# Optimization experiments

Hardware: AMD Instinct MI355X
Metric: run time of the kernel (lower is better)

The kernel has to match this reference:

```python
import jax, jax.numpy as jnp
import numpy as np

THRESHOLD = 0.1  # init kwarg
N_NODES = 8192
N_EDGES = 16384


def setup_inputs() -> dict:
    key = jax.random.key(0)
    k1, k2 = jax.random.split(key)
    node_pos = jax.random.normal(k1, (N_NODES, 2), dtype=jnp.float32)
    edge_index = jax.random.randint(k2, (2, N_EDGES), 0, N_NODES, dtype=jnp.int64)
    return {"node_pos": node_pos, "edge_index": edge_index}


def reference(node_pos, edge_index):
    # edge direction vectors, normalized to unit length (clamped norm as in torch)
    ev = node_pos[edge_index[1]] - node_pos[edge_index[0]]          # [E, 2]
    norms = jnp.linalg.norm(ev, axis=1, keepdims=True)
    ev = ev / jnp.clip(norms, 1e-6)
    # pairwise cosine of angle between every pair of edges: [E, E] gram matrix
    cos = ev @ ev.T
    mask = jnp.abs(cos) > THRESHOLD
    # original loops over i < j only: subtract diagonal hits, halve the rest
    diag_hits = jnp.sum(jnp.abs(jnp.diagonal(cos)) > THRESHOLD)
    n_edges = ev.shape[0]
    count = (jnp.sum(mask) - diag_hits).astype(jnp.float32) * 0.5
    return count / (n_edges * (n_edges - 1) / 2)
```

## Files before the change

kernel.cpp:

```cpp
#include <hip/hip_runtime.h>
#include <math.h>


#define K_BINS 8192
#define NTHR   1024
#define KPT    16
#define PI_F   3.14159265358979323846f
#define A_LO_F 1.4706289056333368f

__global__ __launch_bounds__(256) void angle_kernel(const float* __restrict__ pos,
                                                    const int* __restrict__ eidx,
                                                    float* __restrict__ phi, int E) {
    int i = blockIdx.x * blockDim.x + threadIdx.x;
    if (i >= E) return;
    int s = eidx[i];
    int t = eidx[E + i];
    float dx = pos[2 * t]     - pos[2 * s];
    float dy = pos[2 * t + 1] - pos[2 * s + 1];
    float p;
    if (dx == 0.f && dy == 0.f) {
        p = -1.f;
    } else {
        p = atan2f(dy, dx);
        if (p < 0.f)    p += PI_F;
        if (p >= PI_F)  p -= PI_F;
        if (p < 0.f)    p = 0.f;
    }
    phi[i] = p;
}

__global__ __launch_bounds__(NTHR) void hist_count_kernel(const float* __restrict__ phi,
                                                          float* __restrict__ out, int E) {
    __shared__ unsigned hist[K_BINS];
    __shared__ unsigned wbase[NTHR / 64];
    __shared__ unsigned long long wU[NTHR / 64];
    __shared__ unsigned wND[NTHR / 64];
    __shared__ unsigned s_total;

    int tid  = threadIdx.x;
    int lane = tid & 63;
    int wid  = tid >> 6;
    const float scale = (float)K_BINS / PI_F;

    for (int b = tid; b < K_BINS; b += NTHR) hist[b] = 0u;
    __syncthreads();

    float ph[KPT];
#pragma unroll
    for (int k = 0; k < KPT; ++k) {
        int i = tid + k * NTHR;
        float p = (i < E) ? phi[i] : -1.f;
        ph[k] = p;
        if (p >= 0.f) {
            int b = (int)(p * scale);
            if (b >= K_BINS) b = K_BINS - 1;
            atomicAdd(&hist[b], 1u);
        }
    }
    __syncthreads();

    unsigned h[8];
    unsigned lsum = 0;
    int base = tid * (K_BINS / NTHR);
#pragma unroll
    for (int k = 0; k < 8; ++k) { h[k] = hist[base + k]; lsum += h[k]; }
    unsigned inc = lsum;
    for (int off = 1; off < 64; off <<= 1) {
        unsigned v = __shfl_up(inc, off);
        if (lane >= off) inc += v;
    }
    if (lane == 63) wbase[wid] = inc;
    __syncthreads();
    if (tid < NTHR / 64) {
        unsigned wv = wbase[tid];
        unsigned winc = wv;
        for (int off = 1; off < NTHR / 64; off <<= 1) {
            unsigned v = __shfl_up(winc, off);
            if (tid >= off) winc += v;
        }
        wbase[tid] = winc - wv;
        if (tid == NTHR / 64 - 1) s_total = winc;
    }
    __syncthreads();
    unsigned run = wbase[wid] + (inc - lsum);
#pragma unroll
    for (int k = 0; k < 8; ++k) { hist[base + k] = run; run += h[k]; }
    __syncthreads();

    unsigned total = s_total;
    unsigned long long U = 0;
    unsigned nd = 0;
#pragma unroll
    for (int k = 0; k < KPT; ++k) {
        float p = ph[k];
        if (p < 0.f) continue;
        nd++;
        float lo = p + A_LO_F;
        float hi = p + (PI_F - A_LO_F);
        if (lo >= PI_F) lo -= PI_F;
        if (hi >= PI_F) hi -= PI_F;
        int blo = (int)(lo * scale); if (blo >= K_BINS) blo = K_BINS - 1;
        int bhi = (int)(hi * scale); if (bhi >= K_BINS) bhi = K_BINS - 1;
        unsigned c = (blo <= bhi) ? (hist[bhi] - hist[blo])
                                  : (total - hist[blo] + hist[bhi]);
        U += c;
    }
    for (int off = 32; off > 0; off >>= 1) {
        U  += __shfl_down(U, off);
        nd += __shfl_down(nd, off);
    }
    if (lane == 0) { wU[wid] = U; wND[wid] = nd; }
    __syncthreads();
    if (tid == 0) {
        unsigned long long Ut = 0; unsigned ndt = 0;
        for (int w = 0; w < NTHR / 64; ++w) { Ut += wU[w]; ndt += wND[w]; }
        double nd_d = (double)ndt;
        double pairs_nd  = nd_d * (nd_d - 1.0) * 0.5;
        double band_pairs = (double)Ut * 0.5;
        double count = pairs_nd - band_pairs;
        double denom = (double)E * (double)(E - 1) * 0.5;
        out[0] = (float)(count / denom);
    }
}

extern "C" void kernel_launch(void* const* d_in, const int* in_sizes, int n_in,
                              void* d_out, int out_size, void* d_ws, size_t ws_size,
                              hipStream_t stream) {
    const float* pos  = (const float*)d_in[0];
    const int*   eidx = (const int*)d_in[1];
    int E = in_sizes[1] / 2;

    float* phi = (float*)d_ws;

    angle_kernel<<<(E + 255) / 256, 256, 0, stream>>>(pos, eidx, phi, E);
    hist_count_kernel<<<1, NTHR, 0, stream>>>(phi, (float*)d_out, E);
}
```

Before: 66.16 us.

## Store quantized bin indices and count band pairs per bin instead of per edge

```diff
diff --git a/kernel.cpp b/kernel.cpp
--- a/kernel.cpp
+++ b/kernel.cpp
@@ -3,67 +3,74 @@
 
 
 #define K_BINS 8192
+#define OFF_LO 3835
+#define OFF_HI (K_BINS - OFF_LO)
 #define NTHR   1024
-#define KPT    16
+#define BPT    (K_BINS / NTHR)
 #define PI_F   3.14159265358979323846f
-#define A_LO_F 1.4706289056333368f
 
-__global__ __launch_bounds__(256) void angle_kernel(const float* __restrict__ pos,
-                                                    const int* __restrict__ eidx,
-                                                    float* __restrict__ phi, int E) {
+__global__ __launch_bounds__(64) void bin_kernel(const float* __restrict__ pos,
+                                                 const int* __restrict__ eidx,
+                                                 unsigned short* __restrict__ bins, int E) {
     int i = blockIdx.x * blockDim.x + threadIdx.x;
     if (i >= E) return;
     int s = eidx[i];
     int t = eidx[E + i];
     float dx = pos[2 * t]     - pos[2 * s];
     float dy = pos[2 * t + 1] - pos[2 * s + 1];
-    float p;
+    unsigned short b;
     if (dx == 0.f && dy == 0.f) {
-        p = -1.f;
+        b = 0xFFFFu;
     } else {
-        p = atan2f(dy, dx);
-        if (p < 0.f)    p += PI_F;
-        if (p >= PI_F)  p -= PI_F;
-        if (p < 0.f)    p = 0.f;
+        float p = atan2f(dy, dx);
+        if (p < 0.f)   p += PI_F;
+        int bi = (int)(p * ((float)K_BINS / PI_F));
+        if (bi >= K_BINS) bi -= K_BINS;
+        if (bi < 0) bi = 0;
+        b = (unsigned short)bi;
     }
-    phi[i] = p;
+    bins[i] = b;
 }
 
-__global__ __launch_bounds__(NTHR) void hist_count_kernel(const float* __restrict__ phi,
+__global__ __launch_bounds__(NTHR) void hist_count_kernel(const unsigned short* __restrict__ bins,
                                                           float* __restrict__ out, int E) {
     __shared__ unsigned hist[K_BINS];
     __shared__ unsigned wbase[NTHR / 64];
     __shared__ unsigned long long wU[NTHR / 64];
-    __shared__ unsigned wND[NTHR / 64];
     __shared__ unsigned s_total;
 
     int tid  = threadIdx.x;
     int lane = tid & 63;
     int wid  = tid >> 6;
-    const float scale = (float)K_BINS / PI_F;
 
     for (int b = tid; b < K_BINS; b += NTHR) hist[b] = 0u;
     __syncthreads();
 
-    float ph[KPT];
+    {
+        const uint4* v = (const uint4*)bins;
+        int nvec = E / 8;
 #pragma unroll
-    for (int k = 0; k < KPT; ++k) {
-        int i = tid + k * NTHR;
-        float p = (i < E) ? phi[i] : -1.f;
-        ph[k] = p;
-        if (p >= 0.f) {
-            int b = (int)(p * scale);
-            if (b >= K_BINS) b = K_BINS - 1;
-            atomicAdd(&hist[b], 1u);
+        for (int k = 0; k < 2; ++k) {
+            int idx = tid + k * NTHR;
+            if (idx < nvec) {
+                uint4 w = v[idx];
+                unsigned ws[4] = {w.x, w.y, w.z, w.w};
+#pragma unroll
+                for (int q = 0; q < 4; ++q) {
+                    unsigned lo = ws[q] & 0xFFFFu, hi = ws[q] >> 16;
+                    if (lo != 0xFFFFu) atomicAdd(&hist[lo], 1u);
+                    if (hi != 0xFFFFu) atomicAdd(&hist[hi], 1u);
+                }
+            }
         }
     }
     __syncthreads();
 
-    unsigned h[8];
+    unsigned h[BPT];
     unsigned lsum = 0;
-    int base = tid * (K_BINS / NTHR);
+    int base = tid * BPT;
 #pragma unroll
-    for (int k = 0; k < 8; ++k) { h[k] = hist[base + k]; lsum += h[k]; }
+    for (int k = 0; k < BPT; ++k) { h[k] = hist[base + k]; lsum += h[k]; }
     unsigned inc = lsum;
     for (int off = 1; off < 64; off <<= 1) {
         unsigned v = __shfl_up(inc, off);
@@ -84,40 +91,31 @@
     __syncthreads();
     unsigned run = wbase[wid] + (inc - lsum);
 #pragma unroll
-    for (int k = 0; k < 8; ++k) { hist[base + k] = run; run += h[k]; }
+    for (int k = 0; k < BPT; ++k) { hist[base + k] = run; run += h[k]; }
     __syncthreads();
 
     unsigned total = s_total;
     unsigned long long U = 0;
-    unsigned nd = 0;
 #pragma unroll
-    for (int k = 0; k < KPT; ++k) {
-        float p = ph[k];
-        if (p < 0.f) continue;
-        nd++;
-        float lo = p + A_LO_F;
-        float hi = p + (PI_F - A_LO_F);
-        if (lo >= PI_F) lo -= PI_F;
-        if (hi >= PI_F) hi -= PI_F;
-        int blo = (int)(lo * scale); if (blo >= K_BINS) blo = K_BINS - 1;
-        int bhi = (int)(hi * scale); if (bhi >= K_BINS) bhi = K_BINS - 1;
-        unsigned c = (blo <= bhi) ? (hist[bhi] - hist[blo])
-                                  : (total - hist[blo] + hist[bhi]);
-        U += c;
+    for (int k = 0; k < BPT; ++k) {
+        unsigned c = h[k];
+        if (c) {
+            int b  = base + k;
+            int xm = (b + OFF_LO) & (K_BINS - 1);
+            int ym = (b + OFF_HI) & (K_BINS - 1);
+            unsigned W = (xm < ym) ? (hist[ym] - hist[xm])
+                                   : (total - hist[xm] + hist[ym]);
+            U += (unsigned long long)c * W;
+        }
     }
-    for (int off = 32; off > 0; off >>= 1) {
-        U  += __shfl_down(U, off);
-        nd += __shfl_down(nd, off);
-    }
-    if (lane == 0) { wU[wid] = U; wND[wid] = nd; }
+    for (int off = 32; off > 0; off >>= 1) U += __shfl_down(U, off);
+    if (lane == 0) wU[wid] = U;
     __syncthreads();
     if (tid == 0) {
-        unsigned long long Ut = 0; unsigned ndt = 0;
-        for (int w = 0; w < NTHR / 64; ++w) { Ut += wU[w]; ndt += wND[w]; }
-        double nd_d = (double)ndt;
-        double pairs_nd  = nd_d * (nd_d - 1.0) * 0.5;
-        double band_pairs = (double)Ut * 0.5;
-        double count = pairs_nd - band_pairs;
+        unsigned long long Ut = 0;
+        for (int w = 0; w < NTHR / 64; ++w) Ut += wU[w];
+        double nd = (double)total;
+        double count = nd * (nd - 1.0) * 0.5 - (double)Ut * 0.5;
         double denom = (double)E * (double)(E - 1) * 0.5;
         out[0] = (float)(count / denom);
     }
@@ -130,8 +128,8 @@
     const int*   eidx = (const int*)d_in[1];
     int E = in_sizes[1] / 2;
 
-    float* phi = (float*)d_ws;
+    unsigned short* bins = (unsigned short*)d_ws;
 
-    angle_kernel<<<(E + 255) / 256, 256, 0, stream>>>(pos, eidx, phi, E);
-    hist_count_kernel<<<1, NTHR, 0, stream>>>(phi, (float*)d_out, E);
+    bin_kernel<<<(E + 63) / 64, 64, 0, stream>>>(pos, eidx, bins, E);
+    hist_count_kernel<<<1, NTHR, 0, stream>>>(bins, (float*)d_out, E);
 }
```

Result: faster. 61.58 us (-6.9%).
